# Kernel tuning notes

Measured on AMD Instinct MI355X. Metric: run time of the kernel, lower is better.

The kernel has to match this reference:

```python
import jax, jax.numpy as jnp
import numpy as np

B, T, C = 128, 256, 384
H, D = 6, 64

def setup_inputs() -> dict:
    key = jax.random.key(0)
    ks = jax.random.split(key, 6)
    s = 1.0 / np.sqrt(C)
    return {
        "x": jax.random.normal(ks[0], (B, T, C), dtype=jnp.float32),
        "Wq": jax.random.normal(ks[1], (H, C, D), dtype=jnp.float32) * s,
        "Wk": jax.random.normal(ks[2], (H, C, D), dtype=jnp.float32) * s,
        "Wv": jax.random.normal(ks[3], (H, C, D), dtype=jnp.float32) * s,
        "Wp": jax.random.normal(ks[4], (C, C), dtype=jnp.float32) * s,
        "bp": jnp.zeros((C,), dtype=jnp.float32),
    }

def reference(x, Wq, Wk, Wv, Wp, bp):
    # per-head projections (all heads at once): [B,T,C] x [H,C,D] -> [B,H,T,D]
    q = jnp.einsum("btc,hcd->bhtd", x, Wq)
    k = jnp.einsum("btc,hcd->bhtd", x, Wk)
    v = jnp.einsum("btc,hcd->bhtd", x, Wv)
    scale = 1.0 / jnp.sqrt(jnp.asarray(D, dtype=x.dtype))
    # scores [B,H,T,T], causal mask, softmax
    wei = jnp.einsum("bhqd,bhkd->bhqk", q, k) * scale
    causal = jnp.tril(jnp.ones((T, T), dtype=bool))
    wei = jnp.where(causal, wei, -jnp.inf)
    wei = jax.nn.softmax(wei, axis=-1)
    # dropout layers are identity in eval mode
    out = jnp.einsum("bhqk,bhkd->bhqd", wei, v)
    # concat heads: [B,T,H*D]
    out = out.transpose(0, 2, 1, 3).reshape(B, T, H * D)
    return out @ Wp + bp
```

## Files before the change

kernel.cpp:

```cpp
#include <hip/hip_runtime.h>
#include <stdint.h>


typedef __attribute__((ext_vector_type(8))) short bf16x8;
typedef __attribute__((ext_vector_type(4))) float f32x4;
typedef __attribute__((ext_vector_type(16))) float f32x16;

__device__ __forceinline__ unsigned short f2b(float f) {
    union { float f; unsigned int u; } v; v.f = f;
    unsigned int u = v.u + 0x7fffu + ((v.u >> 16) & 1u);
    return (unsigned short)(u >> 16);
}

__device__ __forceinline__ unsigned int pk2(float lo, float hi) {
    return (unsigned int)f2b(lo) | ((unsigned int)f2b(hi) << 16);
}

__device__ __forceinline__ void gload_lds16(const void* g, void* lds) {
    auto gp = reinterpret_cast<const __attribute__((address_space(1))) uint32_t*>(
        reinterpret_cast<uintptr_t>(g));
    auto lp = reinterpret_cast<__attribute__((address_space(3))) uint32_t*>(
        reinterpret_cast<uintptr_t>(lds));
    __builtin_amdgcn_global_load_lds(gp, lp, 16, 0, 0);
}


__global__ void cvt_x_kernel(const float* __restrict__ x, unsigned short* __restrict__ xb, int n8) {
    int i = blockIdx.x * 256 + threadIdx.x;
    if (i >= n8) return;
    float4 a = ((const float4*)x)[(size_t)i * 2];
    float4 b = ((const float4*)x)[(size_t)i * 2 + 1];
    uint4 o;
    o.x = pk2(a.x, a.y); o.y = pk2(a.z, a.w);
    o.z = pk2(b.x, b.y); o.w = pk2(b.z, b.w);
    ((uint4*)xb)[i] = o;
}

__global__ void cvt_w_kernel(const float* __restrict__ Wq, const float* __restrict__ Wk,
                             const float* __restrict__ Wv, const float* __restrict__ Wp,
                             unsigned short* __restrict__ wt, unsigned short* __restrict__ wpt) {
    int i = blockIdx.x * 256 + threadIdx.x;
    if (i >= 589824) return;
    if (i < 442368) {
        int j = i / 384, c = i - j * 384;
        int p = j / 384, rem = j - p * 384;
        int h = rem >> 6, d = rem & 63;
        const float* W = (p == 0) ? Wq : ((p == 1) ? Wk : Wv);
        wt[i] = f2b(W[(size_t)(h * 384 + c) * 64 + d]);
    } else {
        int i2 = i - 442368;
        int n = i2 / 384, c = i2 - n * 384;
        wpt[i2] = f2b(Wp[(size_t)c * 384 + n]);
    }
}


__global__ __launch_bounds__(256, 4) void gemm_qkv(
    const unsigned short* __restrict__ xb,
    const unsigned short* __restrict__ wt,
    unsigned short* __restrict__ qO,
    unsigned short* __restrict__ kO,
    unsigned short* __restrict__ vO)
{
    extern __shared__ __align__(16) unsigned short smem[];
    unsigned short* AsBase = smem;
    unsigned short* BsBase = smem + 8192;

    const int tid  = threadIdx.x;
    const int lane = tid & 63;
    const int w    = tid >> 6;
    const int wm = w >> 1, wn = w & 1;

    const int flat = blockIdx.y * 9 + blockIdx.x;
    const int swz = (flat & 7) * 288 + (flat >> 3);
    const int bx = swz % 9, by = swz / 9;
    const int col0 = bx * 128;
    const int row0 = by * 128;

    const unsigned short* Abase = xb + (size_t)row0 * 384;
    const unsigned short* Bbase = wt + (size_t)col0 * 384;

    f32x4 acc[4][4];
#pragma unroll
    for (int mf = 0; mf < 4; ++mf)
#pragma unroll
        for (int nf = 0; nf < 4; ++nf)
#pragma unroll
            for (int r = 0; r < 4; ++r) acc[mf][nf][r] = 0.f;

    const int ci0 = tid;
    const int ci1 = tid + 256;
    const unsigned short* aSrc0 = Abase + (size_t)(ci0 >> 2) * 384 + (ci0 & 3) * 8;
    const unsigned short* aSrc1 = Abase + (size_t)(ci1 >> 2) * 384 + (ci1 & 3) * 8;
    const unsigned short* bSrc0 = Bbase + (size_t)(ci0 >> 2) * 384 + (ci0 & 3) * 8;
    const unsigned short* bSrc1 = Bbase + (size_t)(ci1 >> 2) * 384 + (ci1 & 3) * 8;
    const int cb = w * 64;

#define STAGE_QKV(buf, kt)                                                        \
    do {                                                                          \
        const int k0_ = (kt) * 32;                                                \
        gload_lds16(aSrc0 + k0_, AsBase + (buf) * 4096 + (cb + 0) * 8);           \
        gload_lds16(bSrc0 + k0_, BsBase + (buf) * 4096 + (cb + 0) * 8);           \
        gload_lds16(aSrc1 + k0_, AsBase + (buf) * 4096 + (cb + 256) * 8);         \
        gload_lds16(bSrc1 + k0_, BsBase + (buf) * 4096 + (cb + 256) * 8);         \
    } while (0)

    STAGE_QKV(0, 0);
    __syncthreads();

    int cur = 0;
    for (int kt = 0; kt < 12; ++kt) {
        if (kt < 11) STAGE_QKV(cur ^ 1, kt + 1);
        const unsigned short* A = AsBase + cur * 4096;
        const unsigned short* B = BsBase + cur * 4096;
        bf16x8 aF[4], bF[4];
#pragma unroll
        for (int mf = 0; mf < 4; ++mf)
            aF[mf] = *(const bf16x8*)&A[(wm * 64 + mf * 16 + (lane & 15)) * 32 + (lane >> 4) * 8];
#pragma unroll
        for (int nf = 0; nf < 4; ++nf)
            bF[nf] = *(const bf16x8*)&B[(wn * 64 + nf * 16 + (lane & 15)) * 32 + (lane >> 4) * 8];
#pragma unroll
        for (int mf = 0; mf < 4; ++mf)
#pragma unroll
            for (int nf = 0; nf < 4; ++nf)
                acc[mf][nf] = __builtin_amdgcn_mfma_f32_16x16x32_bf16(aF[mf], bF[nf], acc[mf][nf], 0, 0, 0);
        __syncthreads();
        cur ^= 1;
    }
#undef STAGE_QKV

    unsigned short* Ct = smem;
    const int co = tid & 15;
    const int rr = tid >> 4;
    const int colg = col0 + co * 8;
    const int p = colg / 384;
    const int rem = colg - p * 384;
    const int h = rem >> 6;
    const int d = rem & 63;
    unsigned short* dst = (p == 0) ? qO : ((p == 1) ? kO : vO);

#pragma unroll
    for (int ph = 0; ph < 2; ++ph) {
        if (wm == ph) {
#pragma unroll
            for (int mf = 0; mf < 4; ++mf)
#pragma unroll
                for (int nf = 0; nf < 4; ++nf)
#pragma unroll
                    for (int r = 0; r < 4; ++r)
                        Ct[(mf * 16 + (lane >> 4) * 4 + r) * 136 + wn * 64 + nf * 16 + (lane & 15)] =
                            f2b(acc[mf][nf][r]);
        }
        __syncthreads();
#pragma unroll
        for (int it = 0; it < 4; ++it) {
            const int r_loc = it * 16 + rr;
            const int m = row0 + ph * 64 + r_loc;
            const int b = m >> 8, t = m & 255;
            uint4 val = *(const uint4*)&Ct[r_loc * 136 + co * 8];
            *(uint4*)&dst[(size_t)((b * 6 + h) * 256 + t) * 64 + d] = val;
        }
        __syncthreads();
    }
}


__global__ __launch_bounds__(512) void attn_kernel(
    const unsigned short* __restrict__ Qg,
    const unsigned short* __restrict__ Kg,
    const unsigned short* __restrict__ Vg,
    unsigned short* __restrict__ Og)
{
    __shared__ __align__(16) unsigned short Ks[256 * 72];
    __shared__ __align__(16) unsigned short Vs[64 * 264];
    __shared__ __align__(16) unsigned short Ot[8 * 32 * 72];
    const int bh = blockIdx.x;
    const int b = bh / 6, h = bh - b * 6;
    const int tid = threadIdx.x;
    const int lane = tid & 63;
    const int w = tid >> 6;
    const int lo = lane & 31, hi = lane >> 5;

    const unsigned short* kg = Kg + (size_t)bh * 256 * 64;
#pragma unroll
    for (int j = 0; j < 4; ++j) {
        int chunk = tid + 512 * j;
        int key = chunk >> 3, dc = (chunk & 7) * 8;
        *(uint4*)&Ks[key * 72 + dc] = *(const uint4*)&kg[key * 64 + dc];
    }
    {
        const unsigned short* vg = Vg + (size_t)bh * 256 * 64;
        uint32_t* Vs32 = (uint32_t*)Vs;
#pragma unroll
        for (int i = 0; i < 2; ++i) {
            int u = tid + 512 * i;
            int t2 = (u & 31) | ((u >> 8) << 5);
            int dm = (u >> 5) & 7;
            uint4 r0 = *(const uint4*)&vg[(2 * t2 + 0) * 64 + dm * 8];
            uint4 r1 = *(const uint4*)&vg[(2 * t2 + 1) * 64 + dm * 8];
            const unsigned short* e0 = (const unsigned short*)&r0;
            const unsigned short* e1 = (const unsigned short*)&r1;
#pragma unroll
            for (int j = 0; j < 8; ++j)
                Vs32[(dm * 8 + j) * 132 + t2] = (uint32_t)e0[j] | ((uint32_t)e1[j] << 16);
        }
    }
    __syncthreads();

    const int q0 = w * 32;
    const unsigned short* qg = Qg + (size_t)bh * 256 * 64 + (size_t)(q0 + lo) * 64 + hi * 8;
    bf16x8 qF[4];
#pragma unroll
    for (int dc = 0; dc < 4; ++dc) qF[dc] = *(const bf16x8*)(qg + dc * 16);

    float m = -1e30f, ssum = 0.f;
    f32x16 o0, o1;
#pragma unroll
    for (int r = 0; r < 16; ++r) { o0[r] = 0.f; o1[r] = 0.f; }

    for (int kt = 0; kt <= w; ++kt) {
        f32x16 s;
#pragma unroll
        for (int r = 0; r < 16; ++r) s[r] = 0.f;
#pragma unroll
        for (int dc = 0; dc < 4; ++dc) {
            bf16x8 aK = *(const bf16x8*)&Ks[(kt * 32 + lo) * 72 + dc * 16 + hi * 8];
            s = __builtin_amdgcn_mfma_f32_32x32x16_bf16(aK, qF[dc], s, 0, 0, 0);
        }
        float p[16];
        float pmax = -1e30f;
        const bool diag = (kt == w);
#pragma unroll
        for (int r = 0; r < 16; ++r) {
            float sv = s[r] * 0.125f;
            const int keyl = (r & 3) + 8 * (r >> 2) + 4 * hi;
            if (diag && keyl > lo) sv = -1e30f;
            p[r] = sv;
            pmax = fmaxf(pmax, sv);
        }
        pmax = fmaxf(pmax, __shfl_xor(pmax, 32, 64));
        const float mn = fmaxf(m, pmax);
        const float sf = __expf(m - mn);
        m = mn;
        ssum *= sf;
#pragma unroll
        for (int r = 0; r < 16; ++r) { o0[r] *= sf; o1[r] *= sf; }
        float rs = 0.f;
#pragma unroll
        for (int r = 0; r < 16; ++r) { p[r] = __expf(p[r] - m); rs += p[r]; }
        rs += __shfl_xor(rs, 32, 64);
        ssum += rs;

        union { unsigned short u[16]; bf16x8 v[2]; } P;
        {
            float recv[4];
#pragma unroll
            for (int j2 = 0; j2 < 4; ++j2) {
                float sendv = hi ? p[j2] : p[4 + j2];
                recv[j2] = __shfl_xor(sendv, 32, 64);
            }
#pragma unroll
            for (int i = 0; i < 4; ++i) P.u[i]     = f2b(hi ? recv[i] : p[i]);
#pragma unroll
            for (int i = 0; i < 4; ++i) P.u[4 + i] = f2b(hi ? p[4 + i] : recv[i]);
        }
        {
            float recv[4];
#pragma unroll
            for (int j2 = 0; j2 < 4; ++j2) {
                float sendv = hi ? p[8 + j2] : p[12 + j2];
                recv[j2] = __shfl_xor(sendv, 32, 64);
            }
#pragma unroll
            for (int i = 0; i < 4; ++i) P.u[8 + i]  = f2b(hi ? recv[i] : p[8 + i]);
#pragma unroll
            for (int i = 0; i < 4; ++i) P.u[12 + i] = f2b(hi ? p[12 + i] : recv[i]);
        }

#pragma unroll
        for (int kc = 0; kc < 2; ++kc) {
            bf16x8 aV0 = *(const bf16x8*)&Vs[lo * 264 + kt * 32 + kc * 16 + hi * 8];
            o0 = __builtin_amdgcn_mfma_f32_32x32x16_bf16(aV0, P.v[kc], o0, 0, 0, 0);
            bf16x8 aV1 = *(const bf16x8*)&Vs[(32 + lo) * 264 + kt * 32 + kc * 16 + hi * 8];
            o1 = __builtin_amdgcn_mfma_f32_32x32x16_bf16(aV1, P.v[kc], o1, 0, 0, 0);
        }
    }

    const float inv = 1.f / ssum;
    {
        uint32_t* ot32 = (uint32_t*)&Ot[w * 32 * 72];
#pragma unroll
        for (int g = 0; g < 4; ++g) {
            const int dbase0 = 8 * g + 4 * hi;
            uint32_t w0 = pk2(o0[4 * g + 0] * inv, o0[4 * g + 1] * inv);
            uint32_t w1 = pk2(o0[4 * g + 2] * inv, o0[4 * g + 3] * inv);
            int dw = lo * 36 + (dbase0 >> 1);
            ot32[dw] = w0;
            ot32[dw + 1] = w1;
            uint32_t w2 = pk2(o1[4 * g + 0] * inv, o1[4 * g + 1] * inv);
            uint32_t w3 = pk2(o1[4 * g + 2] * inv, o1[4 * g + 3] * inv);
            int dw1 = lo * 36 + ((32 + dbase0) >> 1);
            ot32[dw1] = w2;
            ot32[dw1 + 1] = w3;
        }
    }
    __syncthreads();
    {
        const unsigned short* ot = &Ot[w * 32 * 72];
        const int q = lane >> 1;
        const int half = (lane & 1) * 32;
        unsigned short* og = Og + (size_t)(b * 256 + q0 + q) * 384 + h * 64 + half;
#pragma unroll
        for (int jj = 0; jj < 4; ++jj) {
            uint4 val = *(const uint4*)&ot[q * 72 + half + jj * 8];
            *(uint4*)&og[jj * 8] = val;
        }
    }
}


__global__ __launch_bounds__(256, 4) void gemm_proj(
    const unsigned short* __restrict__ ob,
    const unsigned short* __restrict__ wpt,
    const float* __restrict__ bp,
    float* __restrict__ out)
{
    __shared__ __align__(16) unsigned short As[2][128 * 32];
    __shared__ __align__(16) unsigned short Bs[2][128 * 32];
    const int tid  = threadIdx.x;
    const int lane = tid & 63;
    const int w    = tid >> 6;
    const int wm = w >> 1, wn = w & 1;

    const int flat = blockIdx.y * 3 + blockIdx.x;
    const int swz = (flat & 7) * 96 + (flat >> 3);
    const int bx = swz % 3, by = swz / 3;
    const int col0 = bx * 128;
    const int row0 = by * 128;

    const unsigned short* Abase = ob  + (size_t)row0 * 384;
    const unsigned short* Bbase = wpt + (size_t)col0 * 384;

    f32x4 acc[4][4];
#pragma unroll
    for (int mf = 0; mf < 4; ++mf)
#pragma unroll
        for (int nf = 0; nf < 4; ++nf)
#pragma unroll
            for (int r = 0; r < 4; ++r) acc[mf][nf][r] = 0.f;

    const int ci0 = tid;
    const int ci1 = tid + 256;
    const unsigned short* aSrc0 = Abase + (size_t)(ci0 >> 2) * 384 + (ci0 & 3) * 8;
    const unsigned short* aSrc1 = Abase + (size_t)(ci1 >> 2) * 384 + (ci1 & 3) * 8;
    const unsigned short* bSrc0 = Bbase + (size_t)(ci0 >> 2) * 384 + (ci0 & 3) * 8;
    const unsigned short* bSrc1 = Bbase + (size_t)(ci1 >> 2) * 384 + (ci1 & 3) * 8;
    const int cb = w * 64;

#define STAGE_PRJ(buf, kt)                                                        \
    do {                                                                          \
        const int k0_ = (kt) * 32;                                                \
        gload_lds16(aSrc0 + k0_, (unsigned short*)As[buf] + (cb + 0) * 8);        \
        gload_lds16(bSrc0 + k0_, (unsigned short*)Bs[buf] + (cb + 0) * 8);        \
        gload_lds16(aSrc1 + k0_, (unsigned short*)As[buf] + (cb + 256) * 8);      \
        gload_lds16(bSrc1 + k0_, (unsigned short*)Bs[buf] + (cb + 256) * 8);      \
    } while (0)

    STAGE_PRJ(0, 0);
    __syncthreads();

    int cur = 0;
    for (int kt = 0; kt < 12; ++kt) {
        if (kt < 11) STAGE_PRJ(cur ^ 1, kt + 1);
        const unsigned short* A = As[cur];
        const unsigned short* B = Bs[cur];
        bf16x8 aF[4], bF[4];
#pragma unroll
        for (int mf = 0; mf < 4; ++mf)
            aF[mf] = *(const bf16x8*)&A[(wm * 64 + mf * 16 + (lane & 15)) * 32 + (lane >> 4) * 8];
#pragma unroll
        for (int nf = 0; nf < 4; ++nf)
            bF[nf] = *(const bf16x8*)&B[(wn * 64 + nf * 16 + (lane & 15)) * 32 + (lane >> 4) * 8];
#pragma unroll
        for (int mf = 0; mf < 4; ++mf)
#pragma unroll
            for (int nf = 0; nf < 4; ++nf)
                acc[mf][nf] = __builtin_amdgcn_mfma_f32_16x16x32_bf16(aF[mf], bF[nf], acc[mf][nf], 0, 0, 0);
        __syncthreads();
        cur ^= 1;
    }
#undef STAGE_PRJ

#pragma unroll
    for (int nf = 0; nf < 4; ++nf) {
        const int col = col0 + wn * 64 + nf * 16 + (lane & 15);
        const float bias = bp[col];
#pragma unroll
        for (int mf = 0; mf < 4; ++mf) {
            const int mbase = row0 + wm * 64 + mf * 16 + ((lane >> 4) * 4);
#pragma unroll
            for (int r = 0; r < 4; ++r) {
                const int mrow = mbase + r;
                out[(size_t)mrow * 384 + col] = acc[mf][nf][r] + bias;
            }
        }
    }
}


extern "C" void kernel_launch(void* const* d_in, const int* in_sizes, int n_in,
                              void* d_out, int out_size, void* d_ws, size_t ws_size,
                              hipStream_t stream) {
    const float* x  = (const float*)d_in[0];
    const float* Wq = (const float*)d_in[1];
    const float* Wk = (const float*)d_in[2];
    const float* Wv = (const float*)d_in[3];
    const float* Wp = (const float*)d_in[4];
    const float* bp = (const float*)d_in[5];
    float* out = (float*)d_out;

    char* ws = (char*)d_ws;
    unsigned short* xb  = (unsigned short*)(ws);
    unsigned short* qb  = (unsigned short*)(ws + 25165824);
    unsigned short* kb  = (unsigned short*)(ws + 50331648);
    unsigned short* vb  = (unsigned short*)(ws + 75497472);
    unsigned short* wt  = (unsigned short*)(ws + 100663296);
    unsigned short* wpt = (unsigned short*)(ws + 101548032);

    cvt_x_kernel<<<6144, 256, 0, stream>>>(x, xb, 1572864);
    cvt_w_kernel<<<2304, 256, 0, stream>>>(Wq, Wk, Wv, Wp, wt, wpt);
    gemm_qkv<<<dim3(9, 256), 256, 32768, stream>>>(xb, wt, qb, kb, vb);
    attn_kernel<<<768, 512, 0, stream>>>(qb, kb, vb, xb);
    gemm_proj<<<dim3(3, 256), 256, 0, stream>>>(xb, wpt, bp, out);
}
```

Measured before the change: 123.6 us.

## Triple-buffer GEMM K-loop with vmcnt-based waits instead of syncthreads

Both the QKV and projection GEMMs move from double to triple buffering of LDS tiles. Each step keeps two tiles of async global-to-LDS loads in flight, waits with explicit s_waitcnt vmcnt counts and raw s_barrier, and uses sched_barrier to stop the compiler reordering. This is meant to hide global load latency behind MFMA work. In exchange, LDS use grows from 32KB to 48KB per block and launch bounds drop to 3 blocks per CU, which lowers occupancy.

New measurement: 118.9 us. -3.8%, faster.

```diff
diff --git a/kernel.cpp b/kernel.cpp
--- a/kernel.cpp
+++ b/kernel.cpp
@@ -23,6 +23,8 @@
         reinterpret_cast<uintptr_t>(lds));
     __builtin_amdgcn_global_load_lds(gp, lp, 16, 0, 0);
 }
+
+#define SBAR0() __builtin_amdgcn_sched_barrier(0)
 
 
 __global__ void cvt_x_kernel(const float* __restrict__ x, unsigned short* __restrict__ xb, int n8) {
@@ -55,7 +57,7 @@
 }
 
 
-__global__ __launch_bounds__(256, 4) void gemm_qkv(
+__global__ __launch_bounds__(256, 3) void gemm_qkv(
     const unsigned short* __restrict__ xb,
     const unsigned short* __restrict__ wt,
     unsigned short* __restrict__ qO,
@@ -64,7 +66,7 @@
 {
     extern __shared__ __align__(16) unsigned short smem[];
     unsigned short* AsBase = smem;
-    unsigned short* BsBase = smem + 8192;
+    unsigned short* BsBase = smem + 12288;
 
     const int tid  = threadIdx.x;
     const int lane = tid & 63;
@@ -96,23 +98,17 @@
     const unsigned short* bSrc1 = Bbase + (size_t)(ci1 >> 2) * 384 + (ci1 & 3) * 8;
     const int cb = w * 64;
 
-#define STAGE_QKV(buf, kt)                                                        \
-    do {                                                                          \
-        const int k0_ = (kt) * 32;                                                \
-        gload_lds16(aSrc0 + k0_, AsBase + (buf) * 4096 + (cb + 0) * 8);           \
-        gload_lds16(bSrc0 + k0_, BsBase + (buf) * 4096 + (cb + 0) * 8);           \
-        gload_lds16(aSrc1 + k0_, AsBase + (buf) * 4096 + (cb + 256) * 8);         \
-        gload_lds16(bSrc1 + k0_, BsBase + (buf) * 4096 + (cb + 256) * 8);         \
-    } while (0)
-
-    STAGE_QKV(0, 0);
-    __syncthreads();
-
-    int cur = 0;
-    for (int kt = 0; kt < 12; ++kt) {
-        if (kt < 11) STAGE_QKV(cur ^ 1, kt + 1);
-        const unsigned short* A = AsBase + cur * 4096;
-        const unsigned short* B = BsBase + cur * 4096;
+    auto STAGE = [&](int buf, int kt) {
+        const int k0_ = kt * 32;
+        gload_lds16(aSrc0 + k0_, AsBase + buf * 4096 + (cb + 0) * 8);
+        gload_lds16(bSrc0 + k0_, BsBase + buf * 4096 + (cb + 0) * 8);
+        gload_lds16(aSrc1 + k0_, AsBase + buf * 4096 + (cb + 256) * 8);
+        gload_lds16(bSrc1 + k0_, BsBase + buf * 4096 + (cb + 256) * 8);
+    };
+
+    auto COMPUTE = [&](int buf) {
+        const unsigned short* A = AsBase + buf * 4096;
+        const unsigned short* B = BsBase + buf * 4096;
         bf16x8 aF[4], bF[4];
 #pragma unroll
         for (int mf = 0; mf < 4; ++mf)
@@ -125,10 +121,40 @@
 #pragma unroll
             for (int nf = 0; nf < 4; ++nf)
                 acc[mf][nf] = __builtin_amdgcn_mfma_f32_16x16x32_bf16(aF[mf], bF[nf], acc[mf][nf], 0, 0, 0);
-        __syncthreads();
-        cur ^= 1;
-    }
-#undef STAGE_QKV
+    };
+
+    STAGE(0, 0);
+    STAGE(1, 1);
+    SBAR0();
+    int bufS = 2, bufC = 0;
+    for (int t = 0; t < 10; ++t) {
+        STAGE(bufS, t + 2);
+        bufS = (bufS == 2) ? 0 : bufS + 1;
+        SBAR0();
+        asm volatile("s_waitcnt vmcnt(8)" ::: "memory");
+        SBAR0();
+        __builtin_amdgcn_s_barrier();
+        SBAR0();
+        COMPUTE(bufC);
+        bufC = (bufC == 2) ? 0 : bufC + 1;
+        SBAR0();
+        __builtin_amdgcn_s_barrier();
+        SBAR0();
+    }
+    asm volatile("s_waitcnt vmcnt(4)" ::: "memory");
+    SBAR0();
+    __builtin_amdgcn_s_barrier();
+    SBAR0();
+    COMPUTE(1);
+    SBAR0();
+    __builtin_amdgcn_s_barrier();
+    SBAR0();
+    asm volatile("s_waitcnt vmcnt(0)" ::: "memory");
+    SBAR0();
+    __builtin_amdgcn_s_barrier();
+    SBAR0();
+    COMPUTE(2);
+    __syncthreads();
 
     unsigned short* Ct = smem;
     const int co = tid & 15;
@@ -320,14 +346,14 @@
 }
 
 
-__global__ __launch_bounds__(256, 4) void gemm_proj(
+__global__ __launch_bounds__(256, 3) void gemm_proj(
     const unsigned short* __restrict__ ob,
     const unsigned short* __restrict__ wpt,
     const float* __restrict__ bp,
     float* __restrict__ out)
 {
-    __shared__ __align__(16) unsigned short As[2][128 * 32];
-    __shared__ __align__(16) unsigned short Bs[2][128 * 32];
+    __shared__ __align__(16) unsigned short As[3][128 * 32];
+    __shared__ __align__(16) unsigned short Bs[3][128 * 32];
     const int tid  = threadIdx.x;
     const int lane = tid & 63;
     const int w    = tid >> 6;
@@ -358,23 +384,17 @@
     const unsigned short* bSrc1 = Bbase + (size_t)(ci1 >> 2) * 384 + (ci1 & 3) * 8;
     const int cb = w * 64;
 
-#define STAGE_PRJ(buf, kt)                                                        \
-    do {                                                                          \
-        const int k0_ = (kt) * 32;                                                \
-        gload_lds16(aSrc0 + k0_, (unsigned short*)As[buf] + (cb + 0) * 8);        \
-        gload_lds16(bSrc0 + k0_, (unsigned short*)Bs[buf] + (cb + 0) * 8);        \
-        gload_lds16(aSrc1 + k0_, (unsigned short*)As[buf] + (cb + 256) * 8);      \
-        gload_lds16(bSrc1 + k0_, (unsigned short*)Bs[buf] + (cb + 256) * 8);      \
-    } while (0)
-
-    STAGE_PRJ(0, 0);
-    __syncthreads();
-
-    int cur = 0;
-    for (int kt = 0; kt < 12; ++kt) {
-        if (kt < 11) STAGE_PRJ(cur ^ 1, kt + 1);
-        const unsigned short* A = As[cur];
-        const unsigned short* B = Bs[cur];
+    auto STAGE = [&](int buf, int kt) {
+        const int k0_ = kt * 32;
+        gload_lds16(aSrc0 + k0_, (unsigned short*)As[buf] + (cb + 0) * 8);
+        gload_lds16(bSrc0 + k0_, (unsigned short*)Bs[buf] + (cb + 0) * 8);
+        gload_lds16(aSrc1 + k0_, (unsigned short*)As[buf] + (cb + 256) * 8);
+        gload_lds16(bSrc1 + k0_, (unsigned short*)Bs[buf] + (cb + 256) * 8);
+    };
+
+    auto COMPUTE = [&](int buf) {
+        const unsigned short* A = As[buf];
+        const unsigned short* B = Bs[buf];
         bf16x8 aF[4], bF[4];
 #pragma unroll
         for (int mf = 0; mf < 4; ++mf)
@@ -387,10 +407,39 @@
 #pragma unroll
             for (int nf = 0; nf < 4; ++nf)
                 acc[mf][nf] = __builtin_amdgcn_mfma_f32_16x16x32_bf16(aF[mf], bF[nf], acc[mf][nf], 0, 0, 0);
-        __syncthreads();
-        cur ^= 1;
-    }
-#undef STAGE_PRJ
+    };
+
+    STAGE(0, 0);
+    STAGE(1, 1);
+    SBAR0();
+    int bufS = 2, bufC = 0;
+    for (int t = 0; t < 10; ++t) {
+        STAGE(bufS, t + 2);
+        bufS = (bufS == 2) ? 0 : bufS + 1;
+        SBAR0();
+        asm volatile("s_waitcnt vmcnt(8)" ::: "memory");
+        SBAR0();
+        __builtin_amdgcn_s_barrier();
+        SBAR0();
+        COMPUTE(bufC);
+        bufC = (bufC == 2) ? 0 : bufC + 1;
+        SBAR0();
+        __builtin_amdgcn_s_barrier();
+        SBAR0();
+    }
+    asm volatile("s_waitcnt vmcnt(4)" ::: "memory");
+    SBAR0();
+    __builtin_amdgcn_s_barrier();
+    SBAR0();
+    COMPUTE(1);
+    SBAR0();
+    __builtin_amdgcn_s_barrier();
+    SBAR0();
+    asm volatile("s_waitcnt vmcnt(0)" ::: "memory");
+    SBAR0();
+    __builtin_amdgcn_s_barrier();
+    SBAR0();
+    COMPUTE(2);
 
 #pragma unroll
     for (int nf = 0; nf < 4; ++nf) {
@@ -430,7 +479,7 @@
 
     cvt_x_kernel<<<6144, 256, 0, stream>>>(x, xb, 1572864);
     cvt_w_kernel<<<2304, 256, 0, stream>>>(Wq, Wk, Wv, Wp, wt, wpt);
-    gemm_qkv<<<dim3(9, 256), 256, 32768, stream>>>(xb, wt, qb, kb, vb);
+    gemm_qkv<<<dim3(9, 256), 256, 49152, stream>>>(xb, wt, qb, kb, vb);
     attn_kernel<<<768, 512, 0, stream>>>(qb, kb, vb, xb);
     gemm_proj<<<dim3(3, 256), 256, 0, stream>>>(xb, wpt, bp, out);
 }
```
